# Optimization experiments

Measured on AMD Instinct MI355X. Metric: run time of the kernel, lower is better.

## Reference

```python
import jax, jax.numpy as jnp
import numpy as np

R = 2  # p-norm order, matches init kwarg r=2
NUM_CLASSES = 13  # hardcoded in the original forward


def setup_inputs() -> dict:
    key = jax.random.key(0)
    k1, k2, k3, k4, k5 = jax.random.split(key, 5)
    N = 262144
    inp = jax.random.uniform(k1, (N, NUM_CLASSES), dtype=jnp.float32)
    target = jax.random.randint(k2, (N,), 0, NUM_CLASSES, dtype=jnp.int64)
    s = jax.random.normal(k3, (N, NUM_CLASSES), dtype=jnp.float32)
    C_matrix = jax.random.normal(k4, (N, NUM_CLASSES, NUM_CLASSES), dtype=jnp.float32)
    instance_weights = jax.random.uniform(k5, (N,), dtype=jnp.float32)
    return {"input": inp, "target": target, "s": s, "C_matrix": C_matrix,
            "instance_weights": instance_weights}


def _pnorm(x, r, axis):
    # torch.norm(x, r, dim) for float r: (sum |x|^r)^(1/r)
    return jnp.sum(jnp.abs(x) ** r, axis=axis) ** (1.0 / r)


def reference(input, target, s, C_matrix, instance_weights):
    # one-hot scatter of targets: p[n, target[n]] = 1
    p = jax.nn.one_hot(target, NUM_CLASSES, dtype=input.dtype)  # [N,13]
    # batched matvec: C_matrix [N,13,13] @ p [N,13] -> [N,13]
    z_pe = jnp.einsum('nij,nj->ni', C_matrix, p)
    z_p = s - z_pe
    z_p_norm = _pnorm(z_p, R, axis=1)  # [N]
    z_ye = jnp.einsum('nij,nj->ni', C_matrix, input)
    z_y = s - z_ye
    z_y_norm = _pnorm(z_y, R, axis=1)  # [N]
    # diag(z_y @ z_p^T) == row-wise dot product (original wastefully builds NxN)
    diag = jnp.sum(z_y * z_p, axis=1)  # [N]
    return jnp.sum(z_p_norm - diag / z_y_norm)
```

## Files before the change

kernel.cpp:

```cpp
#include <hip/hip_runtime.h>
#include <hip/hip_bf16.h>

#define NCLS 13
#define ROWS 32
#define BLOCK 256
#define TPB 8
#define C_FLOATS (ROWS * NCLS * NCLS)
#define XS_FLOATS (ROWS * NCLS)
#define C_F4 (C_FLOATS / 4)
#define XS_F4 (XS_FLOATS / 4)

__device__ __forceinline__ void async_cp16(const float* g, float* l) {
    __builtin_amdgcn_global_load_lds(
        (__attribute__((address_space(1))) void*)(const_cast<float*>(g)),
        (__attribute__((address_space(3))) void*)(l),
        16, 0, 0);
}

__device__ __forceinline__ void stage_tile(float* cb, float* xb, float* sb,
                                           const float* Cg, const float* xg,
                                           const float* sg, int tid) {
#pragma unroll
    for (int m = 0; m < 6; ++m) {
        int k = m * BLOCK + tid;
        if (k < C_F4)
            async_cp16(Cg + (size_t)k * 4, cb + (size_t)k * 4);
    }
    if (tid < XS_F4)
        async_cp16(xg + (size_t)tid * 4, xb + (size_t)tid * 4);
    else if (tid >= 128 && tid < 128 + XS_F4)
        async_cp16(sg + (size_t)(tid - 128) * 4, sb + (size_t)(tid - 128) * 4);
}

__global__ __launch_bounds__(BLOCK) void rnorm_kernel(
    const float* __restrict__ input,
    const int* __restrict__ target,
    const float* __restrict__ s,
    const float* __restrict__ C,
    float* __restrict__ out,
    int ntiles)
{
    __shared__ __align__(16) float cbuf[2][C_FLOATS];
    __shared__ __align__(16) float xbuf[2][XS_FLOATS];
    __shared__ __align__(16) float sbuf[2][XS_FLOATS];
    __shared__ float wsum[4];

    const int tid = threadIdx.x;
    const int row = tid >> 3;
    const int q   = tid & 7;

    const int tile0 = blockIdx.x * TPB;
    const int nt = min(TPB, ntiles - tile0);
    float res_acc = 0.0f;

    if (nt > 0) {
        stage_tile(cbuf[0], xbuf[0], sbuf[0],
                   C + (size_t)tile0 * C_FLOATS,
                   input + (size_t)tile0 * XS_FLOATS,
                   s + (size_t)tile0 * XS_FLOATS, tid);
        int t_cur = target[tile0 * ROWS + row];
        asm volatile("s_waitcnt vmcnt(0)" ::: "memory");
        __syncthreads();

        for (int t = 0; t < nt; ++t) {
            const int cur = t & 1;
            const float* cb = cbuf[cur];
            const float* xb = xbuf[cur];
            const float* sb = sbuf[cur];

            int t_next = 0;
            if (t + 1 < nt) {
                const int tile = tile0 + t + 1;
                stage_tile(cbuf[cur ^ 1], xbuf[cur ^ 1], sbuf[cur ^ 1],
                           C + (size_t)tile * C_FLOATS,
                           input + (size_t)tile * XS_FLOATS,
                           s + (size_t)tile * XS_FLOATS, tid);
                t_next = target[tile * ROWS + row];
            }

            float xr[NCLS];
#pragma unroll
            for (int j = 0; j < NCLS; ++j) xr[j] = xb[row * NCLS + j];

            const float* crow = cb + row * (NCLS * NCLS);
            float sp = 0.0f, sy = 0.0f, dd = 0.0f;
            const int tt = t_cur;

            {
                const int i = q;
                float zye = 0.0f, zpe = 0.0f;
#pragma unroll
                for (int j = 0; j < NCLS; ++j) {
                    const float c = crow[i * NCLS + j];
                    zye = fmaf(c, xr[j], zye);
                    if (j == tt) zpe = c;
                }
                const float svi = sb[row * NCLS + i];
                const float zp = svi - zpe, zy = svi - zye;
                sp = fmaf(zp, zp, sp); sy = fmaf(zy, zy, sy); dd = fmaf(zy, zp, dd);
            }
            if (q < 5) {
                const int i = q + 8;
                float zye = 0.0f, zpe = 0.0f;
#pragma unroll
                for (int j = 0; j < NCLS; ++j) {
                    const float c = crow[i * NCLS + j];
                    zye = fmaf(c, xr[j], zye);
                    if (j == tt) zpe = c;
                }
                const float svi = sb[row * NCLS + i];
                const float zp = svi - zpe, zy = svi - zye;
                sp = fmaf(zp, zp, sp); sy = fmaf(zy, zy, sy); dd = fmaf(zy, zp, dd);
            }

            sp += __shfl_xor(sp, 1); sp += __shfl_xor(sp, 2); sp += __shfl_xor(sp, 4);
            sy += __shfl_xor(sy, 1); sy += __shfl_xor(sy, 2); sy += __shfl_xor(sy, 4);
            dd += __shfl_xor(dd, 1); dd += __shfl_xor(dd, 2); dd += __shfl_xor(dd, 4);

            if (q == 0)
                res_acc += sqrtf(sp) - dd / sqrtf(sy);

            if (t + 1 < nt) {
                asm volatile("s_waitcnt vmcnt(0)" ::: "memory");
                __syncthreads();
                t_cur = t_next;
            }
        }
    }

#pragma unroll
    for (int off = 32; off > 0; off >>= 1)
        res_acc += __shfl_down(res_acc, off, 64);

    const int lane = tid & 63;
    const int wid  = tid >> 6;
    if (lane == 0) wsum[wid] = res_acc;
    __syncthreads();
    if (tid == 0)
        atomicAdd(out, wsum[0] + wsum[1] + wsum[2] + wsum[3]);
}

extern "C" void kernel_launch(void* const* d_in, const int* in_sizes, int n_in,
                              void* d_out, int out_size, void* d_ws, size_t ws_size,
                              hipStream_t stream) {
    const float* input  = (const float*)d_in[0];
    const int*   target = (const int*)d_in[1];
    const float* s      = (const float*)d_in[2];
    const float* C      = (const float*)d_in[3];

    float* out = (float*)d_out;
    int N = in_sizes[1];

    hipMemsetAsync(out, 0, sizeof(float) * out_size, stream);

    const int ntiles = N / ROWS;
    const int grid = (ntiles + TPB - 1) / TPB;
    rnorm_kernel<<<grid, BLOCK, 0, stream>>>(input, target, s, C, out, ntiles);
}
```

Before: 48.33 us.

## Stage tiles through registers with single LDS buffer instead of async LDS loads

Replaces the double-buffered async global-to-LDS copies with register prefetch of the next tile followed by an explicit LDS write between two barriers. This halves LDS use, which may allow more resident blocks, and TPB drops from 8 to 4 so the grid doubles. The target-column pick becomes a direct indexed LDS read instead of a select inside the loop. The costs are an extra barrier per tile, higher register pressure from holding six float4 values, and shorter per-block pipelines.

After: 89.17 us. 1.84x slower.

```diff
diff --git a/kernel.cpp b/kernel.cpp
--- a/kernel.cpp
+++ b/kernel.cpp
@@ -4,33 +4,11 @@
 #define NCLS 13
 #define ROWS 32
 #define BLOCK 256
-#define TPB 8
+#define TPB 4
 #define C_FLOATS (ROWS * NCLS * NCLS)
 #define XS_FLOATS (ROWS * NCLS)
 #define C_F4 (C_FLOATS / 4)
 #define XS_F4 (XS_FLOATS / 4)
-
-__device__ __forceinline__ void async_cp16(const float* g, float* l) {
-    __builtin_amdgcn_global_load_lds(
-        (__attribute__((address_space(1))) void*)(const_cast<float*>(g)),
-        (__attribute__((address_space(3))) void*)(l),
-        16, 0, 0);
-}
-
-__device__ __forceinline__ void stage_tile(float* cb, float* xb, float* sb,
-                                           const float* Cg, const float* xg,
-                                           const float* sg, int tid) {
-#pragma unroll
-    for (int m = 0; m < 6; ++m) {
-        int k = m * BLOCK + tid;
-        if (k < C_F4)
-            async_cp16(Cg + (size_t)k * 4, cb + (size_t)k * 4);
-    }
-    if (tid < XS_F4)
-        async_cp16(xg + (size_t)tid * 4, xb + (size_t)tid * 4);
-    else if (tid >= 128 && tid < 128 + XS_F4)
-        async_cp16(sg + (size_t)(tid - 128) * 4, sb + (size_t)(tid - 128) * 4);
-}
 
 __global__ __launch_bounds__(BLOCK) void rnorm_kernel(
     const float* __restrict__ input,
@@ -40,9 +18,9 @@
     float* __restrict__ out,
     int ntiles)
 {
-    __shared__ __align__(16) float cbuf[2][C_FLOATS];
-    __shared__ __align__(16) float xbuf[2][XS_FLOATS];
-    __shared__ __align__(16) float sbuf[2][XS_FLOATS];
+    __shared__ __align__(16) float cb[C_FLOATS];
+    __shared__ __align__(16) float xb[XS_FLOATS];
+    __shared__ __align__(16) float sb[XS_FLOATS];
     __shared__ float wsum[4];
 
     const int tid = threadIdx.x;
@@ -53,30 +31,42 @@
     const int nt = min(TPB, ntiles - tile0);
     float res_acc = 0.0f;
 
+    float4 creg[6];
+    float4 xsreg = make_float4(0.f, 0.f, 0.f, 0.f);
+    int treg = 0;
+
+    auto issue_loads = [&](int tile) {
+        const float4* Cg = (const float4*)(C + (size_t)tile * C_FLOATS);
+#pragma unroll
+        for (int m = 0; m < 6; ++m) {
+            const int k = m * BLOCK + tid;
+            if (m < 5 || k < C_F4) creg[m] = Cg[k];
+        }
+        if (tid < XS_F4)
+            xsreg = ((const float4*)(input + (size_t)tile * XS_FLOATS))[tid];
+        else if (tid >= 128 && tid < 128 + XS_F4)
+            xsreg = ((const float4*)(s + (size_t)tile * XS_FLOATS))[tid - 128];
+        treg = target[tile * ROWS + row];
+        asm volatile("" ::: "memory");
+    };
+    auto write_lds = [&]() {
+#pragma unroll
+        for (int m = 0; m < 6; ++m) {
+            const int k = m * BLOCK + tid;
+            if (m < 5 || k < C_F4) ((float4*)cb)[k] = creg[m];
+        }
+        if (tid < XS_F4) ((float4*)xb)[tid] = xsreg;
+        else if (tid >= 128 && tid < 128 + XS_F4) ((float4*)sb)[tid - 128] = xsreg;
+    };
+
     if (nt > 0) {
-        stage_tile(cbuf[0], xbuf[0], sbuf[0],
-                   C + (size_t)tile0 * C_FLOATS,
-                   input + (size_t)tile0 * XS_FLOATS,
-                   s + (size_t)tile0 * XS_FLOATS, tid);
-        int t_cur = target[tile0 * ROWS + row];
-        asm volatile("s_waitcnt vmcnt(0)" ::: "memory");
+        issue_loads(tile0);
+        write_lds();
         __syncthreads();
+        int t_cur = treg;
 
         for (int t = 0; t < nt; ++t) {
-            const int cur = t & 1;
-            const float* cb = cbuf[cur];
-            const float* xb = xbuf[cur];
-            const float* sb = sbuf[cur];
-
-            int t_next = 0;
-            if (t + 1 < nt) {
-                const int tile = tile0 + t + 1;
-                stage_tile(cbuf[cur ^ 1], xbuf[cur ^ 1], sbuf[cur ^ 1],
-                           C + (size_t)tile * C_FLOATS,
-                           input + (size_t)tile * XS_FLOATS,
-                           s + (size_t)tile * XS_FLOATS, tid);
-                t_next = target[tile * ROWS + row];
-            }
+            if (t + 1 < nt) issue_loads(tile0 + t + 1);
 
             float xr[NCLS];
 #pragma unroll
@@ -84,33 +74,22 @@
 
             const float* crow = cb + row * (NCLS * NCLS);
             float sp = 0.0f, sy = 0.0f, dd = 0.0f;
-            const int tt = t_cur;
 
-            {
-                const int i = q;
-                float zye = 0.0f, zpe = 0.0f;
 #pragma unroll
-                for (int j = 0; j < NCLS; ++j) {
-                    const float c = crow[i * NCLS + j];
-                    zye = fmaf(c, xr[j], zye);
-                    if (j == tt) zpe = c;
+            for (int rep = 0; rep < 2; ++rep) {
+                const int i = q + rep * 8;
+                if (rep == 0 || q < 5) {
+                    float zye = 0.0f;
+#pragma unroll
+                    for (int j = 0; j < NCLS; ++j)
+                        zye = fmaf(crow[i * NCLS + j], xr[j], zye);
+                    const float zpe = crow[i * NCLS + t_cur];
+                    const float svi = sb[row * NCLS + i];
+                    const float zp = svi - zpe, zy = svi - zye;
+                    sp = fmaf(zp, zp, sp);
+                    sy = fmaf(zy, zy, sy);
+                    dd = fmaf(zy, zp, dd);
                 }
-                const float svi = sb[row * NCLS + i];
-                const float zp = svi - zpe, zy = svi - zye;
-                sp = fmaf(zp, zp, sp); sy = fmaf(zy, zy, sy); dd = fmaf(zy, zp, dd);
-            }
-            if (q < 5) {
-                const int i = q + 8;
-                float zye = 0.0f, zpe = 0.0f;
-#pragma unroll
-                for (int j = 0; j < NCLS; ++j) {
-                    const float c = crow[i * NCLS + j];
-                    zye = fmaf(c, xr[j], zye);
-                    if (j == tt) zpe = c;
-                }
-                const float svi = sb[row * NCLS + i];
-                const float zp = svi - zpe, zy = svi - zye;
-                sp = fmaf(zp, zp, sp); sy = fmaf(zy, zy, sy); dd = fmaf(zy, zp, dd);
             }
 
             sp += __shfl_xor(sp, 1); sp += __shfl_xor(sp, 2); sp += __shfl_xor(sp, 4);
@@ -121,9 +100,10 @@
                 res_acc += sqrtf(sp) - dd / sqrtf(sy);
 
             if (t + 1 < nt) {
-                asm volatile("s_waitcnt vmcnt(0)" ::: "memory");
                 __syncthreads();
-                t_cur = t_next;
+                write_lds();
+                __syncthreads();
+                t_cur = treg;
             }
         }
     }
```

## Map one thread per output class with 16-row tiles

Applied to the files above, without the earlier changes.

Shrinks the tile from 32 to 16 rows and assigns 16 threads per row so each of the 13 classes gets its own thread, instead of 8 threads handling one or two classes each. The one-hot term is now a direct indexed LDS read instead of a compare-select loop, and the staging copy is re-laid out for the smaller tile. This cuts per-thread serial work and shrinks LDS use, which may allow more resident blocks. In exchange, 3 of 16 lanes sit idle, each block processes half as much data, so the grid doubles, and the reduction needs one more shuffle step per sum.

Measured after the change: 60.16 us. 1.24x slower.

```diff
diff --git a/kernel.cpp b/kernel.cpp
--- a/kernel.cpp
+++ b/kernel.cpp
@@ -2,7 +2,7 @@
 #include <hip/hip_bf16.h>
 
 #define NCLS 13
-#define ROWS 32
+#define ROWS 16
 #define BLOCK 256
 #define TPB 8
 #define C_FLOATS (ROWS * NCLS * NCLS)
@@ -18,18 +18,21 @@
 }
 
 __device__ __forceinline__ void stage_tile(float* cb, float* xb, float* sb,
-                                           const float* Cg, const float* xg,
-                                           const float* sg, int tid) {
-#pragma unroll
-    for (int m = 0; m < 6; ++m) {
-        int k = m * BLOCK + tid;
-        if (k < C_F4)
-            async_cp16(Cg + (size_t)k * 4, cb + (size_t)k * 4);
-    }
+                                           const float* __restrict__ C,
+                                           const float* __restrict__ input,
+                                           const float* __restrict__ s,
+                                           int tile, int tid) {
+    const float* Cg = C + (size_t)tile * C_FLOATS;
+    async_cp16(Cg + (size_t)tid * 4,         cb + (size_t)tid * 4);
+    async_cp16(Cg + (size_t)(tid + 256) * 4, cb + (size_t)(tid + 256) * 4);
+    if (tid < C_F4 - 512)
+        async_cp16(Cg + (size_t)(tid + 512) * 4, cb + (size_t)(tid + 512) * 4);
     if (tid < XS_F4)
-        async_cp16(xg + (size_t)tid * 4, xb + (size_t)tid * 4);
-    else if (tid >= 128 && tid < 128 + XS_F4)
-        async_cp16(sg + (size_t)(tid - 128) * 4, sb + (size_t)(tid - 128) * 4);
+        async_cp16(input + (size_t)tile * XS_FLOATS + (size_t)tid * 4,
+                   xb + (size_t)tid * 4);
+    else if (tid >= 64 && tid < 64 + XS_F4)
+        async_cp16(s + (size_t)tile * XS_FLOATS + (size_t)(tid - 64) * 4,
+                   sb + (size_t)(tid - 64) * 4);
 }
 
 __global__ __launch_bounds__(BLOCK) void rnorm_kernel(
@@ -46,18 +49,15 @@
     __shared__ float wsum[4];
 
     const int tid = threadIdx.x;
-    const int row = tid >> 3;
-    const int q   = tid & 7;
+    const int row = tid >> 4;
+    const int q   = tid & 15;
 
     const int tile0 = blockIdx.x * TPB;
     const int nt = min(TPB, ntiles - tile0);
     float res_acc = 0.0f;
 
     if (nt > 0) {
-        stage_tile(cbuf[0], xbuf[0], sbuf[0],
-                   C + (size_t)tile0 * C_FLOATS,
-                   input + (size_t)tile0 * XS_FLOATS,
-                   s + (size_t)tile0 * XS_FLOATS, tid);
+        stage_tile(cbuf[0], xbuf[0], sbuf[0], C, input, s, tile0, tid);
         int t_cur = target[tile0 * ROWS + row];
         asm volatile("s_waitcnt vmcnt(0)" ::: "memory");
         __syncthreads();
@@ -70,52 +70,33 @@
 
             int t_next = 0;
             if (t + 1 < nt) {
-                const int tile = tile0 + t + 1;
                 stage_tile(cbuf[cur ^ 1], xbuf[cur ^ 1], sbuf[cur ^ 1],
-                           C + (size_t)tile * C_FLOATS,
-                           input + (size_t)tile * XS_FLOATS,
-                           s + (size_t)tile * XS_FLOATS, tid);
-                t_next = target[tile * ROWS + row];
+                           C, input, s, tile0 + t + 1, tid);
+                t_next = target[(tile0 + t + 1) * ROWS + row];
             }
 
-            float xr[NCLS];
+            float sp = 0.0f, sy = 0.0f, dd = 0.0f;
+            if (q < NCLS) {
+                const float* crow = cb + row * (NCLS * NCLS) + q * NCLS;
+                const float* xrow = xb + row * NCLS;
+                float zye = 0.0f;
 #pragma unroll
-            for (int j = 0; j < NCLS; ++j) xr[j] = xb[row * NCLS + j];
-
-            const float* crow = cb + row * (NCLS * NCLS);
-            float sp = 0.0f, sy = 0.0f, dd = 0.0f;
-            const int tt = t_cur;
-
-            {
-                const int i = q;
-                float zye = 0.0f, zpe = 0.0f;
-#pragma unroll
-                for (int j = 0; j < NCLS; ++j) {
-                    const float c = crow[i * NCLS + j];
-                    zye = fmaf(c, xr[j], zye);
-                    if (j == tt) zpe = c;
-                }
-                const float svi = sb[row * NCLS + i];
+                for (int j = 0; j < NCLS; ++j)
+                    zye = fmaf(crow[j], xrow[j], zye);
+                const float zpe = crow[t_cur];
+                const float svi = sb[row * NCLS + q];
                 const float zp = svi - zpe, zy = svi - zye;
-                sp = fmaf(zp, zp, sp); sy = fmaf(zy, zy, sy); dd = fmaf(zy, zp, dd);
-            }
-            if (q < 5) {
-                const int i = q + 8;
-                float zye = 0.0f, zpe = 0.0f;
-#pragma unroll
-                for (int j = 0; j < NCLS; ++j) {
-                    const float c = crow[i * NCLS + j];
-                    zye = fmaf(c, xr[j], zye);
-                    if (j == tt) zpe = c;
-                }
-                const float svi = sb[row * NCLS + i];
-                const float zp = svi - zpe, zy = svi - zye;
-                sp = fmaf(zp, zp, sp); sy = fmaf(zy, zy, sy); dd = fmaf(zy, zp, dd);
+                sp = zp * zp;
+                sy = zy * zy;
+                dd = zy * zp;
             }
 
-            sp += __shfl_xor(sp, 1); sp += __shfl_xor(sp, 2); sp += __shfl_xor(sp, 4);
-            sy += __shfl_xor(sy, 1); sy += __shfl_xor(sy, 2); sy += __shfl_xor(sy, 4);
-            dd += __shfl_xor(dd, 1); dd += __shfl_xor(dd, 2); dd += __shfl_xor(dd, 4);
+            sp += __shfl_xor(sp, 1); sp += __shfl_xor(sp, 2);
+            sp += __shfl_xor(sp, 4); sp += __shfl_xor(sp, 8);
+            sy += __shfl_xor(sy, 1); sy += __shfl_xor(sy, 2);
+            sy += __shfl_xor(sy, 4); sy += __shfl_xor(sy, 8);
+            dd += __shfl_xor(dd, 1); dd += __shfl_xor(dd, 2);
+            dd += __shfl_xor(dd, 4); dd += __shfl_xor(dd, 8);
 
             if (q == 0)
                 res_acc += sqrtf(sp) - dd / sqrtf(sy);
```
